# Performance work log

Measured on AMD Instinct MI355X. Metric: run time of the kernel, lower is better.

Reference implementation:

```python
import jax, jax.numpy as jnp
import numpy as np

GAMMA = 0.5
BATCH, DIM, UNITS = 16384, 512, 1024


def setup_inputs() -> dict:
    key = jax.random.key(0)
    k1, k2 = jax.random.split(key)
    inputs = jax.random.normal(k1, (BATCH, DIM), dtype=jnp.float32)
    mu = jax.random.normal(k2, (DIM, UNITS), dtype=jnp.float32)
    return {"inputs": inputs, "mu": mu}


def reference(inputs, mu):
    # Squared L2 distance from each input row to each center (column of mu):
    x_sq = jnp.sum(inputs * inputs, axis=1, keepdims=True)        # [B, 1]
    mu_sq = jnp.sum(mu * mu, axis=0, keepdims=True)               # [1, U]
    cross = inputs @ mu                                           # [B, U] GEMM
    l2 = x_sq - 2.0 * cross + mu_sq                                # [B, U]
    return jnp.exp(-GAMMA * l2)
```

## Files before the change

kernel.cpp:

```cpp
#include <hip/hip_runtime.h>

#define BATCH 16384
#define DIM   512
#define UNITS 1024

typedef float v16f __attribute__((ext_vector_type(16)));
#define MFMA_F8(a, b, c) __builtin_amdgcn_mfma_f32_32x32x16_fp8_fp8((a), (b), (c), 0, 0, 0)

static __device__ __forceinline__ long cvt8(const float4 f0, const float4 f1) {
    int lo = __builtin_amdgcn_cvt_pk_fp8_f32(f0.x, f0.y, 0, false);
    lo     = __builtin_amdgcn_cvt_pk_fp8_f32(f0.z, f0.w, lo, true);
    int hi = __builtin_amdgcn_cvt_pk_fp8_f32(f1.x, f1.y, 0, false);
    hi     = __builtin_amdgcn_cvt_pk_fp8_f32(f1.z, f1.w, hi, true);
    return (long)(unsigned)lo | ((long)hi << 32);
}
static __device__ __forceinline__ float dot8(const float4 f0, const float4 f1) {
    return f0.x * f0.x + f0.y * f0.y + f0.z * f0.z + f0.w * f0.w
         + f1.x * f1.x + f1.y * f1.y + f1.z * f1.z + f1.w * f1.w;
}

__global__ __launch_bounds__(512, 4)
void rbf_fused_kernel(const float* __restrict__ in, const float* __restrict__ mu,
                      float* __restrict__ out) {
    __shared__ __attribute__((aligned(16))) unsigned char smem[67072];
    unsigned char* Bs = smem;
    float* musq_red = (float*)(smem + 65536);
    float* musq_l   = (float*)(smem + 66560);

    const int t  = threadIdx.x;
    const int l  = t & 63;
    const int w  = t >> 6;
    const int ln = l & 31;
    const int h  = l >> 5;

    const int b   = blockIdx.x;
    const int xcd = b & 7;
    const int j   = b >> 3;
    const int m0  = (xcd * 8 + (j & 7)) * 256;
    const int n0  = (j >> 3) * 128;

    const float4* ap = (const float4*)(in + (size_t)(m0 + w * 32 + ln) * DIM + h * 8);
    float4 p0a = ap[0], p0b = ap[1];
    float4 p1a = ap[4], p1b = ap[5];

    {
        const int ng = w >> 1;
        const int kq = w & 1;
        const float* msrc = mu + (size_t)(kq * 256 + h * 8) * UNITS + n0 + ng * 32 + ln;
        unsigned char* bdst = Bs + (size_t)(((ng * 32 + kq * 16) * 64) + l) * 8;
        float s = 0.f;
#pragma unroll 4
        for (int kk = 0; kk < 16; kk++) {
            float v[8];
#pragma unroll
            for (int jj = 0; jj < 8; jj++) v[jj] = msrc[(size_t)(kk * 16 + jj) * UNITS];
#pragma unroll
            for (int jj = 0; jj < 8; jj++) s += v[jj] * v[jj];
            *(long*)(bdst + kk * 512) =
                cvt8(make_float4(v[0], v[1], v[2], v[3]),
                     make_float4(v[4], v[5], v[6], v[7]));
        }
        s += __shfl_xor(s, 32, 64);
        if (h == 0) musq_red[(ng * 32 + ln) * 2 + kq] = s;
    }
    __syncthreads();
    if (t < 128) musq_l[t] = -0.5f * (musq_red[t * 2] + musq_red[t * 2 + 1]);
    __syncthreads();

    const long* BsL = (const long*)Bs;
    v16f acc0 = (v16f)0.f, acc1 = (v16f)0.f, acc2 = (v16f)0.f, acc3 = (v16f)0.f;
    float sA = 0.f;

#pragma unroll 2
    for (int i = 0; i < 32; i++) {
        const float4 f0 = (i & 1) ? p1a : p0a;
        const float4 f1 = (i & 1) ? p1b : p0b;
        sA += dot8(f0, f1);
        const long a = cvt8(f0, f1);
        if (i < 30) {
            if (i & 1) { p1a = ap[(i + 2) * 4]; p1b = ap[(i + 2) * 4 + 1]; }
            else       { p0a = ap[(i + 2) * 4]; p0b = ap[(i + 2) * 4 + 1]; }
        }
        const int bo = i * 64 + l;
        const long b0 = BsL[bo];
        const long b1 = BsL[bo + 2048];
        const long b2 = BsL[bo + 4096];
        const long b3 = BsL[bo + 6144];
        acc0 = MFMA_F8(a, b0, acc0);
        acc1 = MFMA_F8(a, b1, acc1);
        acc2 = MFMA_F8(a, b2, acc2);
        acc3 = MFMA_F8(a, b3, acc3);
    }

    sA += __shfl_xor(sA, 32, 64);
    const float xv = -0.5f * sA;

    const float mb0 = musq_l[ln];
    const float mb1 = musq_l[32 + ln];
    const float mb2 = musq_l[64 + ln];
    const float mb3 = musq_l[96 + ln];

    const size_t mrow = m0 + w * 32;
    float* obase = out + n0 + ln;
#pragma unroll
    for (int r = 0; r < 16; r++) {
        const int rl = (r & 3) + 8 * (r >> 2) + 4 * h;
        const float xb = __shfl(xv, rl, 64);
        float* orow = obase + (mrow + rl) * UNITS;
        __builtin_nontemporal_store(__expf(acc0[r] + xb + mb0), orow);
        __builtin_nontemporal_store(__expf(acc1[r] + xb + mb1), orow + 32);
        __builtin_nontemporal_store(__expf(acc2[r] + xb + mb2), orow + 64);
        __builtin_nontemporal_store(__expf(acc3[r] + xb + mb3), orow + 96);
    }
}

extern "C" void kernel_launch(void* const* d_in, const int* in_sizes, int n_in,
                              void* d_out, int out_size, void* d_ws, size_t ws_size,
                              hipStream_t stream) {
    const float* inputs = (const float*)d_in[0];
    const float* mu     = (const float*)d_in[1];
    float* out = (float*)d_out;
    (void)d_ws; (void)ws_size;

    rbf_fused_kernel<<<512, 512, 0, stream>>>(inputs, mu, out);
}
```

Before: 128.0 us.

## Split A fp8 conversion across blocks with producer-consumer flags

Each block now converts a 16-row slice of the input tile to fp8 and computes its row norms, writing them to global workspace and signalling an atomic per-M-tile counter. Blocks then stage their mu slice, spin-wait until all 16 producers for their M tile finish, and run the fp8 MFMA GEMM from the pre-converted global A buffer with smaller 256x64 tiles and 1024 blocks of 256 threads. The goal is to remove the redundant per-block fp32-to-fp8 conversion of A (previously repeated for every N tile) and to raise occupancy through smaller LDS use. It adds a memset launch, a global round trip for A, and a spin-wait that depends on all producer blocks being co-resident.

```diff
diff --git a/kernel.cpp b/kernel.cpp
--- a/kernel.cpp
+++ b/kernel.cpp
@@ -5,27 +5,30 @@
 #define UNITS 1024
 
 typedef float v16f __attribute__((ext_vector_type(16)));
+
 #define MFMA_F8(a, b, c) __builtin_amdgcn_mfma_f32_32x32x16_fp8_fp8((a), (b), (c), 0, 0, 0)
 
-static __device__ __forceinline__ long cvt8(const float4 f0, const float4 f1) {
+static __device__ __forceinline__ int2 cvt8(const float4 f0, const float4 f1) {
     int lo = __builtin_amdgcn_cvt_pk_fp8_f32(f0.x, f0.y, 0, false);
     lo     = __builtin_amdgcn_cvt_pk_fp8_f32(f0.z, f0.w, lo, true);
     int hi = __builtin_amdgcn_cvt_pk_fp8_f32(f1.x, f1.y, 0, false);
     hi     = __builtin_amdgcn_cvt_pk_fp8_f32(f1.z, f1.w, hi, true);
-    return (long)(unsigned)lo | ((long)hi << 32);
+    return make_int2(lo, hi);
 }
 static __device__ __forceinline__ float dot8(const float4 f0, const float4 f1) {
     return f0.x * f0.x + f0.y * f0.y + f0.z * f0.z + f0.w * f0.w
          + f1.x * f1.x + f1.y * f1.y + f1.z * f1.z + f1.w * f1.w;
 }
 
-__global__ __launch_bounds__(512, 4)
-void rbf_fused_kernel(const float* __restrict__ in, const float* __restrict__ mu,
-                      float* __restrict__ out) {
-    __shared__ __attribute__((aligned(16))) unsigned char smem[67072];
+__global__ __launch_bounds__(256, 4)
+void rbf_fused_pc_kernel(const float* __restrict__ in, const float* __restrict__ mu,
+                         unsigned char* __restrict__ A8f, float* __restrict__ xsq,
+                         int* __restrict__ done, float* __restrict__ out) {
+    __shared__ __attribute__((aligned(16))) unsigned char smem[37632];
+    float* ldsA = (float*)smem;
     unsigned char* Bs = smem;
-    float* musq_red = (float*)(smem + 65536);
-    float* musq_l   = (float*)(smem + 66560);
+    float* redX = (float*)(smem + 33024);
+    float* mred = (float*)(smem + 37120);
 
     const int t  = threadIdx.x;
     const int l  = t & 63;
@@ -36,18 +39,57 @@
     const int b   = blockIdx.x;
     const int xcd = b & 7;
     const int j   = b >> 3;
-    const int m0  = (xcd * 8 + (j & 7)) * 256;
-    const int n0  = (j >> 3) * 128;
+    const int mt  = xcd * 8 + (j & 7);
+    const int nt  = j >> 3;
+    const int m0  = mt * 256;
+    const int n0  = nt * 64;
+    const int r0  = m0 + nt * 16;
+    const int c   = r0 >> 5;
+    const int ro  = (nt & 1) * 16;
 
-    const float4* ap = (const float4*)(in + (size_t)(m0 + w * 32 + ln) * DIM + h * 8);
-    float4 p0a = ap[0], p0b = ap[1];
-    float4 p1a = ap[4], p1b = ap[5];
+    {
+        const float4* src = (const float4*)(in + (size_t)r0 * DIM);
+        float4* l4 = (float4*)ldsA;
+#pragma unroll
+        for (int i = 0; i < 8; i++) {
+            const int f = i * 256 + t;
+            l4[(f >> 7) * 129 + (f & 127)] = src[f];
+        }
+    }
+    __syncthreads();
+
+    {
+        const int kw = t >> 3, sub = t & 7;
+        const int hh = sub & 1, rq = sub >> 1;
+#pragma unroll
+        for (int i = 0; i < 4; i++) {
+            const int rloc = rq * 4 + i;
+            const float* p = ldsA + rloc * 516 + kw * 16 + hh * 8;
+            float4 f0 = *(const float4*)p;
+            float4 f1 = *(const float4*)(p + 4);
+            redX[rloc * 64 + kw * 2 + hh] = dot8(f0, f1);
+            *(int2*)(A8f + (((size_t)c * 32 + kw) * 64 + hh * 32 + ro + rloc) * 8)
+                = cvt8(f0, f1);
+        }
+    }
+    __syncthreads();
+
+    if (t < 16) {
+        float a = 0.f;
+#pragma unroll
+        for (int i = 0; i < 64; i++) a += redX[t * 64 + i];
+        xsq[r0 + t] = a;
+    }
+    __syncthreads();
+    if (t == 0)
+        __hip_atomic_fetch_add(done + mt, 1, __ATOMIC_RELEASE,
+                               __HIP_MEMORY_SCOPE_AGENT);
 
     {
         const int ng = w >> 1;
         const int kq = w & 1;
         const float* msrc = mu + (size_t)(kq * 256 + h * 8) * UNITS + n0 + ng * 32 + ln;
-        unsigned char* bdst = Bs + (size_t)(((ng * 32 + kq * 16) * 64) + l) * 8;
+        unsigned char* bdst = Bs + (((ng * 32 + kq * 16) * 64) + l) * 8;
         float s = 0.f;
 #pragma unroll 4
         for (int kk = 0; kk < 16; kk++) {
@@ -56,61 +98,53 @@
             for (int jj = 0; jj < 8; jj++) v[jj] = msrc[(size_t)(kk * 16 + jj) * UNITS];
 #pragma unroll
             for (int jj = 0; jj < 8; jj++) s += v[jj] * v[jj];
-            *(long*)(bdst + kk * 512) =
+            *(int2*)(bdst + kk * 512) =
                 cvt8(make_float4(v[0], v[1], v[2], v[3]),
                      make_float4(v[4], v[5], v[6], v[7]));
         }
         s += __shfl_xor(s, 32, 64);
-        if (h == 0) musq_red[(ng * 32 + ln) * 2 + kq] = s;
+        if (h == 0) mred[(ng * 32 + ln) * 2 + kq] = s;
     }
     __syncthreads();
-    if (t < 128) musq_l[t] = -0.5f * (musq_red[t * 2] + musq_red[t * 2 + 1]);
+
+    if (t == 0) {
+        while (__hip_atomic_load(done + mt, __ATOMIC_RELAXED,
+                                 __HIP_MEMORY_SCOPE_AGENT) < 16)
+            __builtin_amdgcn_s_sleep(4);
+        (void)__hip_atomic_load(done + mt, __ATOMIC_ACQUIRE,
+                                __HIP_MEMORY_SCOPE_AGENT);
+    }
     __syncthreads();
 
     const long* BsL = (const long*)Bs;
-    v16f acc0 = (v16f)0.f, acc1 = (v16f)0.f, acc2 = (v16f)0.f, acc3 = (v16f)0.f;
-    float sA = 0.f;
+    const long* Bp  = BsL + l;
+#pragma unroll
+    for (int p = 0; p < 2; p++) {
+        const int mbase = m0 + w * 64 + p * 32;
+        const long* Af = (const long*)A8f + (size_t)(mbase >> 5) * 2048 + l;
 
-#pragma unroll 2
-    for (int i = 0; i < 32; i++) {
-        const float4 f0 = (i & 1) ? p1a : p0a;
-        const float4 f1 = (i & 1) ? p1b : p0b;
-        sA += dot8(f0, f1);
-        const long a = cvt8(f0, f1);
-        if (i < 30) {
-            if (i & 1) { p1a = ap[(i + 2) * 4]; p1b = ap[(i + 2) * 4 + 1]; }
-            else       { p0a = ap[(i + 2) * 4]; p0b = ap[(i + 2) * 4 + 1]; }
+        v16f acc0 = (v16f)0.f, acc1 = (v16f)0.f;
+#pragma unroll 4
+        for (int kw = 0; kw < 32; kw++) {
+            long a  = Af[kw * 64];
+            long b0 = Bp[kw * 64];
+            long b1 = Bp[2048 + kw * 64];
+            acc0 = MFMA_F8(a, b0, acc0);
+            acc1 = MFMA_F8(a, b1, acc1);
         }
-        const int bo = i * 64 + l;
-        const long b0 = BsL[bo];
-        const long b1 = BsL[bo + 2048];
-        const long b2 = BsL[bo + 4096];
-        const long b3 = BsL[bo + 6144];
-        acc0 = MFMA_F8(a, b0, acc0);
-        acc1 = MFMA_F8(a, b1, acc1);
-        acc2 = MFMA_F8(a, b2, acc2);
-        acc3 = MFMA_F8(a, b3, acc3);
-    }
 
-    sA += __shfl_xor(sA, 32, 64);
-    const float xv = -0.5f * sA;
-
-    const float mb0 = musq_l[ln];
-    const float mb1 = musq_l[32 + ln];
-    const float mb2 = musq_l[64 + ln];
-    const float mb3 = musq_l[96 + ln];
-
-    const size_t mrow = m0 + w * 32;
-    float* obase = out + n0 + ln;
+        const float xv  = -0.5f * xsq[mbase + ln];
+        const float mb0 = -0.5f * (mred[ln * 2] + mred[ln * 2 + 1]);
+        const float mb1 = -0.5f * (mred[(32 + ln) * 2] + mred[(32 + ln) * 2 + 1]);
+        float* obase = out + n0 + ln;
 #pragma unroll
-    for (int r = 0; r < 16; r++) {
-        const int rl = (r & 3) + 8 * (r >> 2) + 4 * h;
-        const float xb = __shfl(xv, rl, 64);
-        float* orow = obase + (mrow + rl) * UNITS;
-        __builtin_nontemporal_store(__expf(acc0[r] + xb + mb0), orow);
-        __builtin_nontemporal_store(__expf(acc1[r] + xb + mb1), orow + 32);
-        __builtin_nontemporal_store(__expf(acc2[r] + xb + mb2), orow + 64);
-        __builtin_nontemporal_store(__expf(acc3[r] + xb + mb3), orow + 96);
+        for (int r = 0; r < 16; r++) {
+            const int rl = (r & 3) + 8 * (r >> 2) + 4 * h;
+            const float xb = __shfl(xv, rl, 64);
+            float* orow = obase + (size_t)(mbase + rl) * UNITS;
+            __builtin_nontemporal_store(__expf(acc0[r] + xb + mb0), orow);
+            __builtin_nontemporal_store(__expf(acc1[r] + xb + mb1), orow + 32);
+        }
     }
 }
 
@@ -120,7 +154,13 @@
     const float* inputs = (const float*)d_in[0];
     const float* mu     = (const float*)d_in[1];
     float* out = (float*)d_out;
-    (void)d_ws; (void)ws_size;
 
-    rbf_fused_kernel<<<512, 512, 0, stream>>>(inputs, mu, out);
+    char* ws = (char*)d_ws;
+    unsigned char* A8f = (unsigned char*)ws;
+    float* xsq = (float*)(ws + (size_t)BATCH * DIM);
+    int*   done = (int*)(ws + (size_t)BATCH * DIM + BATCH * 4);
+
+    hipMemsetAsync(done, 0, 64 * sizeof(int), stream);
+    rbf_fused_pc_kernel<<<1024, 256, 0, stream>>>(
+        inputs, mu, A8f, xsq, done, out);
 }
```

After: 157.3 us. +22.9%, slower.
